# Optimization experiments

Measured on AMD Instinct MI355X. Metric: run time of the kernel, lower is better.

The kernel has to match this reference:

```python
import jax, jax.numpy as jnp
import numpy as np

INPUT_SIZE = 256
NUM_LABELS = 50
L = NUM_LABELS + 1  # internal label count incl. pad label (index L-1)
B, T = 64, 256


def setup_inputs() -> dict:
    key = jax.random.key(0)
    k = jax.random.split(key, 8)
    inp = {
        "input": jax.random.normal(k[0], (B, T, INPUT_SIZE), dtype=jnp.float32),
        "mask": jnp.ones((B, T), dtype=jnp.float32),
        "target": jax.random.randint(k[1], (B, T), 0, NUM_LABELS),
        # state_nn: Linear(input_size, L)
        "state_W": jax.random.normal(k[2], (INPUT_SIZE, L), dtype=jnp.float32) * 0.05,
        "state_b": jnp.zeros((L,), dtype=jnp.float32),
        # trans_nn: Linear(input_size, L*L) (bigram=True)
        "trans_W": jax.random.normal(k[3], (INPUT_SIZE, L * L), dtype=jnp.float32) * 0.05,
        "trans_b": jnp.zeros((L * L,), dtype=jnp.float32),
    }
    return inp


def _energy(x, mask, state_W, state_b, trans_W, trans_b):
    # out_s: [B,T,L]  (unary scores), out_t: [B,T,L,L] (bigram transitions)
    out_s = jnp.einsum("bti,il->btl", x, state_W) + state_b
    out_t = (jnp.einsum("bti,io->bto", x, trans_W) + trans_b).reshape(
        x.shape[0], x.shape[1], L, L
    )
    energy = out_t + out_s[:, :, None, :]  # [B,T,L,L]
    return energy * mask[:, :, None, None]


def reference(input, mask, target, state_W, state_b, trans_W, trans_b):
    """ChainCRF.loss: -log p(target | input) per batch element, shape [B]."""
    energy = _energy(input, mask, state_W, state_b, trans_W, trans_b)
    e_t = jnp.transpose(energy, (1, 0, 2, 3))  # [T,B,L,L]
    tgt_t = target.T                            # [T,B]
    msk_t = mask.T                              # [T,B]
    bidx = jnp.arange(input.shape[0])

    # t = 0: start from pad label (index L-1)
    partition0 = e_t[0][:, L - 1, :]                       # [B,L]
    tgt0 = e_t[0][bidx, L - 1, tgt_t[0]]                   # [B]

    def step(carry, xs):
        part, tgt_e, prev = carry
        curr, tgt, m = xs  # curr [B,L,L], tgt [B], m [B]
        part_new = jax.nn.logsumexp(curr + part[:, :, None], axis=1)
        part = part + (part_new - part) * m[:, None]
        tgt_e = tgt_e + curr[bidx, prev, tgt]
        return (part, tgt_e, tgt), None

    (part, tgt_e, _), _ = jax.lax.scan(
        step, (partition0, tgt0, tgt_t[0]), (e_t[1:], tgt_t[1:], msk_t[1:])
    )
    return jax.nn.logsumexp(part, axis=1) - tgt_e
```

## Files before the change

kernel.cpp:

```cpp
#include <hip/hip_runtime.h>
#include <hip/hip_bf16.h>

#define B_    64
#define T_    256
#define K_    256
#define L_    51
#define LL_   2601
#define RS_   64
#define NG_   3328
#define PST_  4096
#define MT_   128
#define NT_   128
#define TS_   72

typedef __bf16 bf16x8 __attribute__((ext_vector_type(8)));
typedef float  f32x4  __attribute__((ext_vector_type(4)));
typedef unsigned int u32x4 __attribute__((ext_vector_type(4)));
typedef u32x4 __attribute__((may_alias)) u32x4_a;
typedef unsigned long long ull;
typedef ull __attribute__((may_alias)) ull_a;

static __device__ __forceinline__ bf16x8 as_bf16x8(u32x4 u) {
    return __builtin_bit_cast(bf16x8, u);
}
static __device__ __forceinline__ unsigned short bf16bits(float x) {
    return __builtin_bit_cast(unsigned short, __float2bfloat16(x));
}
static __device__ __forceinline__ ull pack4(f32x4 a) {
    return (ull)bf16bits(a[0]) | ((ull)bf16bits(a[1]) << 16) |
           ((ull)bf16bits(a[2]) << 32) | ((ull)bf16bits(a[3]) << 48);
}
static __device__ __forceinline__ void gld_lds16(const void* g, void* l) {
    __builtin_amdgcn_global_load_lds(
        (const __attribute__((address_space(1))) unsigned int*)g,
        (__attribute__((address_space(3))) unsigned int*)l, 16, 0, 0);
}

#define DPP_STEP(v, OP, CTRL)                                                   \
    {                                                                           \
        int _x = __builtin_bit_cast(int, v);                                    \
        float _o = __builtin_bit_cast(                                          \
            float, __builtin_amdgcn_update_dpp(_x, _x, CTRL, 0xF, 0xF, true));  \
        v = OP(v, _o);                                                          \
    }
static __device__ __forceinline__ float addf(float a, float b) { return a + b; }

__global__ __launch_bounds__(256) void prep_all(
    const float* __restrict__ trans_W, const float* __restrict__ trans_b,
    const float* __restrict__ state_W, const float* __restrict__ state_b,
    const float* __restrict__ x,
    __hip_bfloat16* __restrict__ Wt, float* __restrict__ bias,
    __hip_bfloat16* __restrict__ xb, __hip_bfloat16* __restrict__ P, int Tc)
{
    __shared__ __align__(16) __hip_bfloat16 Wl[52 * 258];
    const int blk = blockIdx.x, tid = threadIdx.x;

    if (blk < 64) {
        const int i = blk;
        if (i < L_) {
            const int jp = tid & 63, kk = tid >> 6;
            if (jp < 52) {
                for (int k = kk; k < K_; k += 4) {
                    float v = 0.f;
                    if (jp < L_) v = trans_W[(size_t)k * LL_ + i * L_ + jp] +
                                     state_W[k * L_ + jp];
                    Wl[jp * 258 + k] = __float2bfloat16(v);
                }
            }
            __syncthreads();
            for (int idx = tid; idx < 52 * 32; idx += 256) {
                const int j = idx >> 5, c = idx & 31;
                const unsigned int* row = (const unsigned int*)&Wl[j * 258];
                u32x4 v;
                v[0] = row[c * 4 + 0]; v[1] = row[c * 4 + 1];
                v[2] = row[c * 4 + 2]; v[3] = row[c * 4 + 3];
                *(u32x4*)(Wt + (size_t)((j << 6) + i) * K_ + c * 8) = v;
            }
        } else {
            const u32x4 z = {};
            for (int idx = tid; idx < 52 * 32; idx += 256) {
                const int j = idx >> 5, c = idx & 31;
                *(u32x4*)(Wt + (size_t)((j << 6) + i) * K_ + c * 8) = z;
            }
        }
        if (tid < 52) {
            const int j = tid;
            bias[(j << 6) + i] =
                (i < L_ && j < L_) ? trans_b[i * L_ + j] + state_b[j] : 0.f;
        }
    } else if (blk < 64 + 1024) {
        const int n4 = B_ * T_ * K_ / 4;
        const float4* x4 = (const float4*)x;
        ushort4* xb4 = (ushort4*)xb;
        for (int idx = (blk - 64) * 256 + tid; idx < n4; idx += 1024 * 256) {
            float4 v = x4[idx];
            ushort4 o;
            o.x = bf16bits(v.x); o.y = bf16bits(v.y);
            o.z = bf16bits(v.z); o.w = bf16bits(v.w);
            xb4[idx] = o;
        }
    } else {
        const int per = (PST_ - NG_) / 8;
        const int tot = B_ * Tc * per;
        u32x4* P16 = (u32x4*)P;
        const u32x4 z = {};
        for (int idx = (blk - 1088) * 256 + tid; idx < tot; idx += 1024 * 256) {
            const int m = idx / per;
            const int q = idx - m * per;
            P16[(size_t)m * (PST_ / 8) + (NG_ / 8) + q] = z;
        }
    }
}

__global__ __launch_bounds__(256) void gemm_energy(
    const __hip_bfloat16* __restrict__ xb,
    const __hip_bfloat16* __restrict__ Wt,
    const float* __restrict__ bias,
    const float* __restrict__ mask,
    __hip_bfloat16* __restrict__ P,
    int t0, int Tc, int TcShift)
{
    __shared__ __align__(16) __hip_bfloat16 As[MT_ * 64];
    __shared__ __align__(16) __hip_bfloat16 Bs[NT_ * 64];

    const int tid  = threadIdx.x;
    const int lane = tid & 63;
    const int wv   = tid >> 6;
    const int quad = lane >> 4;
    const int l16  = lane & 15;
    const int m0 = blockIdx.y * MT_;
    const int n0 = blockIdx.x * NT_;
    const int mrow0 = (wv >> 1) * 64;
    const int ncol0 = (wv & 1) * 64;

    f32x4 acc[4][4] = {};

    for (int kp = 0; kp < 4; ++kp) {
        if (kp) __syncthreads();
#pragma unroll
        for (int it = 0; it < 4; ++it) {
            const int s = it * 256 + tid;
            const int r = s >> 3;
            const int c = (lane & 7) ^ (r & 7);
            const int ma = m0 + r;
            const int rg = (ma >> TcShift) * T_ + t0 + (ma & (Tc - 1));
            gld_lds16((const char*)xb + (size_t)rg * 512 + kp * 128 + c * 16,
                      (char*)As + it * 4096 + wv * 1024);
            gld_lds16((const char*)Wt + (size_t)(n0 + r) * 512 + kp * 128 + c * 16,
                      (char*)Bs + it * 4096 + wv * 1024);
        }
        asm volatile("s_waitcnt vmcnt(0)" ::: "memory");
        __syncthreads();

        const u32x4_a* Av = (const u32x4_a*)As;
        const u32x4_a* Bv = (const u32x4_a*)Bs;
#pragma unroll
        for (int kk = 0; kk < 2; ++kk) {
            bf16x8 af[4], bfr[4];
#pragma unroll
            for (int f = 0; f < 4; ++f) {
                const int ra = mrow0 + f * 16 + l16;
                af[f]  = as_bf16x8(Av[ra * 8 + ((kk * 4 + quad) ^ (ra & 7))]);
                const int rb = ncol0 + f * 16 + l16;
                bfr[f] = as_bf16x8(Bv[rb * 8 + ((kk * 4 + quad) ^ (rb & 7))]);
            }
#pragma unroll
            for (int mf = 0; mf < 4; ++mf)
#pragma unroll
                for (int nf = 0; nf < 4; ++nf)
                    acc[mf][nf] = __builtin_amdgcn_mfma_f32_16x16x32_bf16(
                        af[mf], bfr[nf], acc[mf][nf], 0, 0, 0);
        }
    }

    const int jcol = (n0 + ncol0) >> 6;
    const bool jok = jcol < L_;
    float bv[4]; bool ok[4]; int ncol[4], ii[4];
#pragma unroll
    for (int nf = 0; nf < 4; ++nf) {
        const int n = n0 + ncol0 + nf * 16 + l16;
        ncol[nf] = n;
        ii[nf]   = nf * 16 + l16;
        ok[nf]   = jok && (ii[nf] < L_);
        bv[nf]   = bias[n];
    }
#pragma unroll
    for (int mf = 0; mf < 4; ++mf) {
#pragma unroll
        for (int r = 0; r < 4; ++r) {
            const int m  = m0 + mrow0 + mf * 16 + quad * 4 + r;
            const int bb = m >> TcShift;
            const int tl = m & (Tc - 1);
            const int t  = t0 + tl;
            const float mval = mask[bb * T_ + t];
            const bool idm = (mval == 0.f) && (t != 0);
            __hip_bfloat16* prow = P + (size_t)m * PST_;
#pragma unroll
            for (int nf = 0; nf < 4; ++nf) {
                float v;
                if (idm) v = (ok[nf] && ii[nf] == jcol) ? 1.f : 0.f;
                else     v = ok[nf] ? __expf((acc[mf][nf][r] + bv[nf]) * mval) : 0.f;
                prow[ncol[nf]] = __float2bfloat16(v);
            }
        }
    }
}

__global__ __launch_bounds__(256) void prod_quad(
    const __hip_bfloat16* __restrict__ P,
    __hip_bfloat16* __restrict__ Q,
    int Tc)
{
    __shared__ u32x4 Sm[4][512];
    __shared__ __align__(16) unsigned short T1t[64 * TS_];
    __shared__ __align__(16) unsigned short T3t[64 * TS_];
    __shared__ __align__(16) unsigned short W2t[64 * TS_];
    __shared__ __align__(16) unsigned short W4b[64 * TS_];

    const int tid  = threadIdx.x;
    const int wv   = tid >> 6;
    const int lane = tid & 63;
    const int quad = lane >> 4;
    const int l16  = lane & 15;
    const int bq = blockIdx.x;
    const int Tq = Tc >> 2;
    const int b  = bq / Tq;
    const int tq = bq - b * Tq;
    const __hip_bfloat16* tile0 = P + (size_t)(b * Tc + tq * 4) * PST_;

#pragma unroll
    for (int q = 0; q < 8; ++q) {
        const int idx  = q * 4 + wv;
        const int tile = idx >> 3;
        const int part = idx & 7;
        const int slot = part * 64 + lane;
        const int r    = slot >> 3;
        const int csrc = (slot & 7) ^ (r & 7);
        gld_lds16((const char*)(tile0 + (size_t)tile * PST_) + (r * 8 + csrc) * 16,
                  (char*)&Sm[tile][part * 64]);
    }

    u32x4 idf[2];
    {
        const int e = l16 & 7;
        const unsigned int bits = (e & 1) ? 0x3F800000u : 0x3F80u;
#pragma unroll
        for (int par = 0; par < 2; ++par) {
            u32x4 v = {};
            if (quad == (l16 >> 3) + par * 2) v[e >> 1] = bits;
            idf[par] = v;
        }
    }

    const int ra = wv * 16 + l16;
    const f32x4 z = {};
    asm volatile("s_waitcnt vmcnt(0)" ::: "memory");
    __syncthreads();

#pragma unroll
    for (int tt = 0; tt < 2; ++tt) {
        const u32x4* S = Sm[tt * 2];
        bf16x8 a0 = as_bf16x8(S[ra * 8 + (quad ^ (ra & 7))]);
        bf16x8 a1 = as_bf16x8(S[ra * 8 + ((4 + quad) ^ (ra & 7))]);
        unsigned short* dst = tt ? T3t : T1t;
#pragma unroll
        for (int nf = 0; nf < 4; ++nf) {
            f32x4 d = __builtin_amdgcn_mfma_f32_16x16x32_bf16(
                (nf >> 1) ? a1 : a0, as_bf16x8(idf[nf & 1]), z, 0, 0, 0);
            *(ull_a*)(dst + (nf * 16 + l16) * TS_ + wv * 16 + quad * 4) = pack4(d);
        }
    }
    __syncthreads();

    {
        bf16x8 a2[2], a3[2];
#pragma unroll
        for (int ks = 0; ks < 2; ++ks) {
            a2[ks] = as_bf16x8(Sm[1][ra * 8 + ((ks * 4 + quad) ^ (ra & 7))]);
            a3[ks] = as_bf16x8(*(const u32x4_a*)(T3t + ra * TS_ + ks * 32 + quad * 8));
        }
#pragma unroll
        for (int nf = 0; nf < 4; ++nf) {
            const int rb = nf * 16 + l16;
            f32x4 u = z, v = z;
#pragma unroll
            for (int ks = 0; ks < 2; ++ks) {
                bf16x8 bU = as_bf16x8(*(const u32x4_a*)(T1t + rb * TS_ + ks * 32 + quad * 8));
                bf16x8 bV = as_bf16x8(Sm[3][rb * 8 + ((ks * 4 + quad) ^ (rb & 7))]);
                u = __builtin_amdgcn_mfma_f32_16x16x32_bf16(a2[ks], bU, u, 0, 0, 0);
                v = __builtin_amdgcn_mfma_f32_16x16x32_bf16(a3[ks], bV, v, 0, 0, 0);
            }
            *(ull_a*)(W2t + rb * TS_ + wv * 16 + quad * 4) = pack4(u);
            *(ull_a*)(W4b + rb * TS_ + wv * 16 + quad * 4) = pack4(v);
        }
    }
    __syncthreads();

    {
        bf16x8 aw[2];
#pragma unroll
        for (int ks = 0; ks < 2; ++ks)
            aw[ks] = as_bf16x8(*(const u32x4_a*)(W2t + ra * TS_ + ks * 32 + quad * 8));
#pragma unroll
        for (int nf = 0; nf < 4; ++nf) {
            const int rb = nf * 16 + l16;
            f32x4 d = z;
#pragma unroll
            for (int ks = 0; ks < 2; ++ks) {
                bf16x8 bw = as_bf16x8(*(const u32x4_a*)(W4b + rb * TS_ + ks * 32 + quad * 8));
                d = __builtin_amdgcn_mfma_f32_16x16x32_bf16(aw[ks], bw, d, 0, 0, 0);
            }
            *(ull_a*)(T1t + rb * TS_ + wv * 16 + quad * 4) = pack4(d);
        }
    }
    __syncthreads();

    u32x4* qout = (u32x4*)(Q + (size_t)bq * PST_);
#pragma unroll
    for (int c = tid; c < 512; c += 256) {
        const int row = c >> 3;
        const int pos = c & 7;
        qout[row * 8 + pos] = *(const u32x4_a*)(T1t + row * TS_ + pos * 8);
    }
}

__global__ __launch_bounds__(128, 1) void scan_q(
    const __hip_bfloat16* __restrict__ Q,
    const __hip_bfloat16* __restrict__ P,
    const int* __restrict__ target, const float* __restrict__ mask,
    float* __restrict__ p_ws, float* __restrict__ ls_ws,
    float* __restrict__ tgt_ws, float* __restrict__ out,
    int t0q, int Tq, int Tqtot)
{
    __shared__ __align__(16) unsigned short p_arr[64];
    __shared__ float tgt_sh;

    const int b    = blockIdx.x;
    const int tid  = threadIdx.x;
    const int wv   = tid >> 6;
    const int lane = tid & 63;
    const int quad = lane >> 4;
    const int l16  = lane & 15;
    const int t0 = t0q << 2, Tc = Tq << 2;

    float pv[4] = {0.f, 0.f, 0.f, 0.f};
    float logscale = 0.f;

    if (wv == 0) {
        if (t0q == 0) {
            p_arr[lane] = (lane == L_ - 1) ? (unsigned short)0x3F80 : (unsigned short)0;
        } else {
#pragma unroll
            for (int f = 0; f < 4; ++f) pv[f] = p_ws[b * 64 + f * 16 + l16];
            logscale = ls_ws[b];
            p_arr[quad * 16 + l16] = bf16bits(pv[quad]);
        }
        asm volatile("s_waitcnt lgkmcnt(0)" ::: "memory");

        int off[8];
#pragma unroll
        for (int f = 0; f < 4; ++f)
#pragma unroll
            for (int ks = 0; ks < 2; ++ks)
                off[f * 2 + ks] = (f * 16 + l16) * 8 + ks * 4 + quad;

        const u32x4* gp = (const u32x4*)Q + (size_t)b * Tq * (PST_ / 8);
        const u32x4_a* pa = (const u32x4_a*)p_arr;

        u32x4 s0[8], s1[8], s2[8], s3[8];
        auto fetch = [&](u32x4 (&st)[8], int tl) {
            const u32x4* g = gp + (size_t)tl * (PST_ / 8);
#pragma unroll
            for (int q = 0; q < 8; ++q) st[q] = g[off[q]];
        };
        fetch(s0, 0);
        if (1 < Tq) fetch(s1, 1);
        if (2 < Tq) fetch(s2, 2);
        if (3 < Tq) fetch(s3, 3);

        auto step = [&](u32x4 (&st)[8], int tl) {
            bf16x8 a0 = as_bf16x8(pa[quad]);
            bf16x8 a1 = as_bf16x8(pa[4 + quad]);
            const f32x4 z = {};
            f32x4 ae[4], ao[4];
#pragma unroll
            for (int f = 0; f < 4; ++f) {
                ae[f] = __builtin_amdgcn_mfma_f32_16x16x32_bf16(a0, as_bf16x8(st[f * 2 + 0]), z, 0, 0, 0);
                ao[f] = __builtin_amdgcn_mfma_f32_16x16x32_bf16(a1, as_bf16x8(st[f * 2 + 1]), z, 0, 0, 0);
            }
#pragma unroll
            for (int f = 0; f < 4; ++f) pv[f] = ae[f][0] + ao[f][0];

            if (((tl & 1) == 1) || (tl == Tq - 1)) {
                float mx = fmaxf(fmaxf(pv[0], pv[1]), fmaxf(pv[2], pv[3]));
                DPP_STEP(mx, fmaxf, 0xB1);
                DPP_STEP(mx, fmaxf, 0x4E);
                DPP_STEP(mx, fmaxf, 0x124);
                DPP_STEP(mx, fmaxf, 0x128);
                const float inv = 1.f / mx;
                logscale += __logf(mx);
#pragma unroll
                for (int f = 0; f < 4; ++f) pv[f] *= inv;
            }
            p_arr[quad * 16 + l16] = bf16bits(pv[quad]);
            asm volatile("s_waitcnt lgkmcnt(0)" ::: "memory");
        };

        for (int tl = 0; tl < Tq; tl += 4) {
            step(s0, tl);
            if (tl + 4 < Tq) fetch(s0, tl + 4);
            if (tl + 1 < Tq) { step(s1, tl + 1); if (tl + 5 < Tq) fetch(s1, tl + 5); }
            if (tl + 2 < Tq) { step(s2, tl + 2); if (tl + 6 < Tq) fetch(s2, tl + 6); }
            if (tl + 3 < Tq) { step(s3, tl + 3); if (tl + 7 < Tq) fetch(s3, tl + 7); }
        }
    } else {
        float s = 0.f;
        for (int tl = lane; tl < Tc; tl += 64) {
            const int t = t0 + tl;
            const int j = target[b * T_ + t];
            const int i = (t == 0) ? (L_ - 1) : target[b * T_ + t - 1];
            const float m = (t == 0) ? 1.f : mask[b * T_ + t];
            if (m != 0.f) {
                const float pval =
                    __bfloat162float(P[(size_t)(b * Tc + tl) * PST_ + j * RS_ + i]);
                s += __logf(pval);
            }
        }
#pragma unroll
        for (int d = 1; d < 64; d <<= 1) s += __shfl_xor(s, d);
        if (lane == 0) {
            const float tot = (t0 == 0) ? s : tgt_ws[b] + s;
            tgt_ws[b] = tot;
            tgt_sh = tot;
        }
    }
    __syncthreads();

    if (wv == 0) {
        if (t0q + Tq == Tqtot) {
            float s = pv[0] + pv[1] + pv[2] + pv[3];
            DPP_STEP(s, addf, 0xB1);
            DPP_STEP(s, addf, 0x4E);
            DPP_STEP(s, addf, 0x124);
            DPP_STEP(s, addf, 0x128);
            if (lane == 0) out[b] = logscale + __logf(s) - tgt_sh;
        } else {
            if (quad == 0) {
#pragma unroll
                for (int f = 0; f < 4; ++f) p_ws[b * 64 + f * 16 + l16] = pv[f];
            }
            if (lane == 0) ls_ws[b] = logscale;
        }
    }
}

extern "C" void kernel_launch(void* const* d_in, const int* in_sizes, int n_in,
                              void* d_out, int out_size, void* d_ws, size_t ws_size,
                              hipStream_t stream)
{
    (void)in_sizes; (void)n_in; (void)out_size;
    const float* x       = (const float*)d_in[0];
    const float* mask    = (const float*)d_in[1];
    const int*   target  = (const int*)d_in[2];
    const float* state_W = (const float*)d_in[3];
    const float* state_b = (const float*)d_in[4];
    const float* trans_W = (const float*)d_in[5];
    const float* trans_b = (const float*)d_in[6];
    float* out = (float*)d_out;

    char* ws = (char*)d_ws;
    size_t off = 0;
    auto alloc = [&](size_t bytes) -> void* {
        void* p = ws + off;
        off = (off + bytes + 255) & ~(size_t)255;
        return p;
    };

    __hip_bfloat16* Wt   = (__hip_bfloat16*)alloc((size_t)NG_ * K_ * 2);
    float*          bias = (float*)alloc((size_t)NG_ * 4);
    __hip_bfloat16* xb   = (__hip_bfloat16*)alloc((size_t)B_ * T_ * K_ * 2);
    float*          p_ws = (float*)alloc((size_t)B_ * 64 * 4);
    float*          ls   = (float*)alloc((size_t)B_ * 4);
    float*          tgte = (float*)alloc((size_t)B_ * 4);
    const size_t fixed = off;

    int Tc = 256;
    while (Tc > 4 && fixed + (size_t)Tc * B_ * PST_ * 2 * 5 / 4 + 512 > ws_size) Tc >>= 1;
    __hip_bfloat16* P = (__hip_bfloat16*)alloc((size_t)Tc * B_ * PST_ * 2);
    __hip_bfloat16* Q = (__hip_bfloat16*)alloc((size_t)(Tc / 4) * B_ * PST_ * 2);
    int TcShift = 0;
    while ((1 << TcShift) < Tc) ++TcShift;

    prep_all<<<dim3(2112), 256, 0, stream>>>(
        trans_W, trans_b, state_W, state_b, x, Wt, bias, xb, P, Tc);

    for (int t0 = 0; t0 < T_; t0 += Tc) {
        gemm_energy<<<dim3(NG_ / NT_, (B_ * Tc) / MT_), 256, 0, stream>>>(
            xb, Wt, bias, mask, P, t0, Tc, TcShift);
        prod_quad<<<dim3(B_ * (Tc / 4)), 256, 0, stream>>>(P, Q, Tc);
        scan_q<<<dim3(B_), 128, 0, stream>>>(Q, P, target, mask, p_ws, ls, tgte, out,
                                             t0 / 4, Tc / 4, T_ / 4);
    }
}
```

Before: 215.3 us.

## Stage GEMM epilogue in LDS for coalesced stores; shrink prod_quad LDS

The gemm_energy epilogue now writes bf16 results into a rotated LDS tile, then stores each row to P as coalesced 16-byte vectors instead of scattered 2-byte writes. The grid axes are swapped so consecutive blocks walk along M, and launch bounds request more resident blocks. prod_quad replaces its four padded transpose buffers with two XOR-swizzled ones and reuses the Sm input buffers for intermediates, which cuts LDS use so more blocks fit per CU. This adds extra barriers and an LDS round trip, and the register caps could cause spills.

```diff
diff --git a/kernel.cpp b/kernel.cpp
--- a/kernel.cpp
+++ b/kernel.cpp
@@ -11,7 +11,6 @@
 #define PST_  4096
 #define MT_   128
 #define NT_   128
-#define TS_   72
 
 typedef __bf16 bf16x8 __attribute__((ext_vector_type(8)));
 typedef float  f32x4  __attribute__((ext_vector_type(4)));
@@ -19,6 +18,7 @@
 typedef u32x4 __attribute__((may_alias)) u32x4_a;
 typedef unsigned long long ull;
 typedef ull __attribute__((may_alias)) ull_a;
+typedef unsigned short ushort_a __attribute__((may_alias));
 
 static __device__ __forceinline__ bf16x8 as_bf16x8(u32x4 u) {
     return __builtin_bit_cast(bf16x8, u);
@@ -112,7 +112,7 @@
     }
 }
 
-__global__ __launch_bounds__(256) void gemm_energy(
+__global__ __launch_bounds__(256, 5) void gemm_energy(
     const __hip_bfloat16* __restrict__ xb,
     const __hip_bfloat16* __restrict__ Wt,
     const float* __restrict__ bias,
@@ -128,8 +128,8 @@
     const int wv   = tid >> 6;
     const int quad = lane >> 4;
     const int l16  = lane & 15;
-    const int m0 = blockIdx.y * MT_;
-    const int n0 = blockIdx.x * NT_;
+    const int m0 = blockIdx.x * MT_;
+    const int n0 = blockIdx.y * NT_;
     const int mrow0 = (wv >> 1) * 64;
     const int ncol0 = (wv & 1) * 64;
 
@@ -172,14 +172,15 @@
                         af[mf], bfr[nf], acc[mf][nf], 0, 0, 0);
         }
     }
-
+    __syncthreads();
+
+    char* E = (char*)As;
     const int jcol = (n0 + ncol0) >> 6;
     const bool jok = jcol < L_;
-    float bv[4]; bool ok[4]; int ncol[4], ii[4];
+    float bv[4]; bool ok[4]; int ii[4];
 #pragma unroll
     for (int nf = 0; nf < 4; ++nf) {
         const int n = n0 + ncol0 + nf * 16 + l16;
-        ncol[nf] = n;
         ii[nf]   = nf * 16 + l16;
         ok[nf]   = jok && (ii[nf] < L_);
         bv[nf]   = bias[n];
@@ -188,34 +189,52 @@
     for (int mf = 0; mf < 4; ++mf) {
 #pragma unroll
         for (int r = 0; r < 4; ++r) {
-            const int m  = m0 + mrow0 + mf * 16 + quad * 4 + r;
+            const int ml = mrow0 + mf * 16 + quad * 4 + r;
+            const int m  = m0 + ml;
             const int bb = m >> TcShift;
             const int tl = m & (Tc - 1);
             const int t  = t0 + tl;
             const float mval = mask[bb * T_ + t];
             const bool idm = (mval == 0.f) && (t != 0);
-            __hip_bfloat16* prow = P + (size_t)m * PST_;
+            char* erow = E + ml * 256;
+            const int rot = (ml * 8) & 255;
 #pragma unroll
             for (int nf = 0; nf < 4; ++nf) {
                 float v;
                 if (idm) v = (ok[nf] && ii[nf] == jcol) ? 1.f : 0.f;
                 else     v = ok[nf] ? __expf((acc[mf][nf][r] + bv[nf]) * mval) : 0.f;
-                prow[ncol[nf]] = __float2bfloat16(v);
-            }
-        }
-    }
-}
-
-__global__ __launch_bounds__(256) void prod_quad(
+                const int nloc = ncol0 + nf * 16 + l16;
+                *(ushort_a*)(erow + ((nloc * 2 + rot) & 255)) = bf16bits(v);
+            }
+        }
+    }
+    __syncthreads();
+
+#pragma unroll
+    for (int it2 = 0; it2 < 8; ++it2) {
+        const int idx = it2 * 256 + tid;
+        const int ml = idx >> 4, c = idx & 15;
+        const char* erow = E + ml * 256;
+        const int rot = (ml * 8) & 255;
+        const ull lo = *(const ull_a*)(erow + ((c * 16 + rot) & 255));
+        const ull hi = *(const ull_a*)(erow + ((c * 16 + 8 + rot) & 255));
+        u32x4 v;
+        v[0] = (unsigned int)lo; v[1] = (unsigned int)(lo >> 32);
+        v[2] = (unsigned int)hi; v[3] = (unsigned int)(hi >> 32);
+        *(u32x4*)(P + (size_t)(m0 + ml) * PST_ + n0 + c * 8) = v;
+    }
+}
+
+__global__ __launch_bounds__(256, 3) void prod_quad(
     const __hip_bfloat16* __restrict__ P,
     __hip_bfloat16* __restrict__ Q,
     int Tc)
 {
     __shared__ u32x4 Sm[4][512];
-    __shared__ __align__(16) unsigned short T1t[64 * TS_];
-    __shared__ __align__(16) unsigned short T3t[64 * TS_];
-    __shared__ __align__(16) unsigned short W2t[64 * TS_];
-    __shared__ __align__(16) unsigned short W4b[64 * TS_];
+    __shared__ __align__(16) unsigned short Tb[2][64 * 64];
+
+    unsigned short* W2t = (unsigned short*)&Sm[0][0];
+    unsigned short* W4b = (unsigned short*)&Sm[2][0];
 
     const int tid  = threadIdx.x;
     const int wv   = tid >> 6;
@@ -252,6 +271,14 @@
         }
     }
 
+    auto twr = [&](unsigned short* buf, int rb, int colb, ull v) {
+        *(ull_a*)((char*)buf + rb * 128 + ((colb + 16 * (rb & 7)) & 127)) = v;
+    };
+    auto trd = [&](const unsigned short* buf, int r, int colb) -> u32x4 {
+        return *(const u32x4_a*)((char*)buf + r * 128 + ((colb + 16 * (r & 7)) & 127));
+    };
+    const int wcol = wv * 32 + quad * 8;
+
     const int ra = wv * 16 + l16;
     const f32x4 z = {};
     asm volatile("s_waitcnt vmcnt(0)" ::: "memory");
@@ -262,12 +289,11 @@
         const u32x4* S = Sm[tt * 2];
         bf16x8 a0 = as_bf16x8(S[ra * 8 + (quad ^ (ra & 7))]);
         bf16x8 a1 = as_bf16x8(S[ra * 8 + ((4 + quad) ^ (ra & 7))]);
-        unsigned short* dst = tt ? T3t : T1t;
 #pragma unroll
         for (int nf = 0; nf < 4; ++nf) {
             f32x4 d = __builtin_amdgcn_mfma_f32_16x16x32_bf16(
                 (nf >> 1) ? a1 : a0, as_bf16x8(idf[nf & 1]), z, 0, 0, 0);
-            *(ull_a*)(dst + (nf * 16 + l16) * TS_ + wv * 16 + quad * 4) = pack4(d);
+            twr(Tb[tt], nf * 16 + l16, wcol, pack4(d));
         }
     }
     __syncthreads();
@@ -277,21 +303,28 @@
 #pragma unroll
         for (int ks = 0; ks < 2; ++ks) {
             a2[ks] = as_bf16x8(Sm[1][ra * 8 + ((ks * 4 + quad) ^ (ra & 7))]);
-            a3[ks] = as_bf16x8(*(const u32x4_a*)(T3t + ra * TS_ + ks * 32 + quad * 8));
-        }
+            a3[ks] = as_bf16x8(trd(Tb[1], ra, ks * 64 + quad * 16));
+        }
+        ull w2v[4], w4v[4];
 #pragma unroll
         for (int nf = 0; nf < 4; ++nf) {
             const int rb = nf * 16 + l16;
             f32x4 u = z, v = z;
 #pragma unroll
             for (int ks = 0; ks < 2; ++ks) {
-                bf16x8 bU = as_bf16x8(*(const u32x4_a*)(T1t + rb * TS_ + ks * 32 + quad * 8));
+                bf16x8 bU = as_bf16x8(trd(Tb[0], rb, ks * 64 + quad * 16));
                 bf16x8 bV = as_bf16x8(Sm[3][rb * 8 + ((ks * 4 + quad) ^ (rb & 7))]);
                 u = __builtin_amdgcn_mfma_f32_16x16x32_bf16(a2[ks], bU, u, 0, 0, 0);
                 v = __builtin_amdgcn_mfma_f32_16x16x32_bf16(a3[ks], bV, v, 0, 0, 0);
             }
-            *(ull_a*)(W2t + rb * TS_ + wv * 16 + quad * 4) = pack4(u);
-            *(ull_a*)(W4b + rb * TS_ + wv * 16 + quad * 4) = pack4(v);
+            w2v[nf] = pack4(u);
+            w4v[nf] = pack4(v);
+        }
+        __syncthreads();
+#pragma unroll
+        for (int nf = 0; nf < 4; ++nf) {
+            twr(W2t, nf * 16 + l16, wcol, w2v[nf]);
+            twr(W4b, nf * 16 + l16, wcol, w4v[nf]);
         }
     }
     __syncthreads();
@@ -300,18 +333,23 @@
         bf16x8 aw[2];
 #pragma unroll
         for (int ks = 0; ks < 2; ++ks)
-            aw[ks] = as_bf16x8(*(const u32x4_a*)(W2t + ra * TS_ + ks * 32 + quad * 8));
+            aw[ks] = as_bf16x8(trd(W2t, ra, ks * 64 + quad * 16));
+        ull mv[4];
 #pragma unroll
         for (int nf = 0; nf < 4; ++nf) {
             const int rb = nf * 16 + l16;
             f32x4 d = z;
 #pragma unroll
             for (int ks = 0; ks < 2; ++ks) {
-                bf16x8 bw = as_bf16x8(*(const u32x4_a*)(W4b + rb * TS_ + ks * 32 + quad * 8));
+                bf16x8 bw = as_bf16x8(trd(W4b, rb, ks * 64 + quad * 16));
                 d = __builtin_amdgcn_mfma_f32_16x16x32_bf16(aw[ks], bw, d, 0, 0, 0);
             }
-            *(ull_a*)(T1t + rb * TS_ + wv * 16 + quad * 4) = pack4(d);
-        }
+            mv[nf] = pack4(d);
+        }
+        __syncthreads();
+#pragma unroll
+        for (int nf = 0; nf < 4; ++nf)
+            twr(Tb[0], nf * 16 + l16, wcol, mv[nf]);
     }
     __syncthreads();
 
@@ -320,7 +358,7 @@
     for (int c = tid; c < 512; c += 256) {
         const int row = c >> 3;
         const int pos = c & 7;
-        qout[row * 8 + pos] = *(const u32x4_a*)(T1t + row * TS_ + pos * 8);
+        qout[row * 8 + pos] = trd(Tb[0], row, pos * 16);
     }
 }
 
@@ -495,7 +533,7 @@
         trans_W, trans_b, state_W, state_b, x, Wt, bias, xb, P, Tc);
 
     for (int t0 = 0; t0 < T_; t0 += Tc) {
-        gemm_energy<<<dim3(NG_ / NT_, (B_ * Tc) / MT_), 256, 0, stream>>>(
+        gemm_energy<<<dim3((B_ * Tc) / MT_, NG_ / NT_), 256, 0, stream>>>(
             xb, Wt, bias, mask, P, t0, Tc, TcShift);
         prod_quad<<<dim3(B_ * (Tc / 4)), 256, 0, stream>>>(P, Q, Tc);
         scan_q<<<dim3(B_), 128, 0, stream>>>(Q, P, target, mask, p_ws, ls, tgte, out,
```

Measured after the change: 292.3 us. 1.36x slower.
